# Optimization experiments

Hardware: AMD Instinct MI355X
Metric: run time of the kernel (lower is better)

## Reference

```python
import jax, jax.numpy as jnp
import numpy as np

NUM_HEADS = 6
KEY_DIM = 16
D_HEAD = 32  # attn_ratio(2) * key_dim(16)


def conv1x1_bn(x, W, scale, bias):
    # 1x1 conv (no bias) + folded BatchNorm (eval mode) as per-channel affine.
    y = jnp.einsum('oi,bihw->bohw', W, x)
    return y * scale[None, :, None, None] + bias[None, :, None, None]


def setup_inputs() -> dict:
    key = jax.random.key(0)
    ks = jax.random.split(key, 16)
    B, C, H, W = 4, 384, 48, 48
    dim_s = C // 4  # 96
    nh_kd = NUM_HEADS * KEY_DIM  # 96
    dh = NUM_HEADS * D_HEAD      # 192

    def w(k, o, i):
        return jax.random.normal(k, (o, i), dtype=jnp.float32) / np.sqrt(i)

    return {
        'xx': jax.random.normal(ks[0], (B, C, H, W), dtype=jnp.float32),
        'Wq': w(ks[1], nh_kd, dim_s),
        'q_scale': jax.random.uniform(ks[2], (nh_kd,), dtype=jnp.float32, minval=0.5, maxval=1.5),
        'q_bias': 0.1 * jax.random.normal(ks[3], (nh_kd,), dtype=jnp.float32),
        'Wk': w(ks[4], nh_kd, C),
        'k_scale': jax.random.uniform(ks[5], (nh_kd,), dtype=jnp.float32, minval=0.5, maxval=1.5),
        'k_bias': 0.1 * jax.random.normal(ks[6], (nh_kd,), dtype=jnp.float32),
        'Wv': w(ks[7], dh, C),
        'v_scale': jax.random.uniform(ks[8], (dh,), dtype=jnp.float32, minval=0.5, maxval=1.5),
        'v_bias': 0.1 * jax.random.normal(ks[9], (dh,), dtype=jnp.float32),
        'Wp': w(ks[10], dim_s, dh),
        'p_scale': jax.random.uniform(ks[11], (dim_s,), dtype=jnp.float32, minval=0.5, maxval=1.5),
        'p_bias': 0.1 * jax.random.normal(ks[12], (dim_s,), dtype=jnp.float32),
        'Wo': w(ks[13], C, dim_s),
        'o_scale': jax.random.uniform(ks[14], (C,), dtype=jnp.float32, minval=0.5, maxval=1.5),
        'o_bias': 0.1 * jax.random.normal(ks[15], (C,), dtype=jnp.float32),
    }


def reference(xx, Wq, q_scale, q_bias, Wk, k_scale, k_bias, Wv, v_scale, v_bias,
              Wp, p_scale, p_bias, Wo, o_scale, o_bias):
    B, C, H, W = xx.shape
    dim_s = C // 4
    N = H * W
    x = xx[:, 3 * dim_s:]  # last channel split -> query stream [B, dim_s, H, W]

    q = conv1x1_bn(x, Wq, q_scale, q_bias)                    # [B, nh_kd, H, W]
    q = q.reshape(B, NUM_HEADS, KEY_DIM, N).transpose(0, 1, 3, 2)  # [B,h,N,kd]
    k = conv1x1_bn(xx, Wk, k_scale, k_bias).reshape(B, NUM_HEADS, KEY_DIM, N)  # [B,h,kd,N]
    v = conv1x1_bn(xx, Wv, v_scale, v_bias).reshape(B, NUM_HEADS, D_HEAD, N)   # [B,h,d,N]

    # NOTE: original forward never applies key_dim**-0.5 scaling -- faithful to that.
    attn = jax.nn.softmax(jnp.einsum('bhnk,bhkm->bhnm', q, k), axis=-1)  # [B,h,N,N]
    out = jnp.einsum('bhnm,bhdm->bhdn', attn, v)                         # [B,h,d,N]
    out = out.reshape(B, NUM_HEADS * D_HEAD, H, W)

    out = conv1x1_bn(jax.nn.relu(out), Wp, p_scale, p_bias)  # [B, dim_s, H, W]
    xres = x + out  # drop_path=0 -> identity
    y = jax.nn.relu(conv1x1_bn(xres, Wo, o_scale, o_bias))   # [B, C, H, W]
    return y
```

## Files before the change

kernel.cpp:

```cpp
#include <hip/hip_runtime.h>
#include <hip/hip_bf16.h>
#include <math.h>

#define BB 4
#define CIN 384
#define NHD 6
#define KDIM 16
#define DHEAD 32
#define NPOS 2304
#define DIMS 96
#define DHTOT 192

constexpr size_t OFF_WT1 = 0;
constexpr size_t OFF_WT2 = OFF_WT1 + 384 * 384;
constexpr size_t OFF_WT3 = OFF_WT2 + 192 * 96;
constexpr size_t OFF_SC1 = OFF_WT3 + 96 * 384;
constexpr size_t OFF_BS1 = OFF_SC1 + 384;
constexpr size_t OFF_SC2 = OFF_BS1 + 384;
constexpr size_t OFF_BS2 = OFF_SC2 + 96;
constexpr size_t OFF_SC3 = OFF_BS2 + 96;
constexpr size_t OFF_BS3 = OFF_SC3 + 384;

constexpr size_t OFFB_Q  = (OFF_BS3 + 384) * 4;
constexpr size_t OFFB_K  = OFFB_Q + (size_t)BB * NHD * NPOS * KDIM * 2;
constexpr size_t OFFB_V  = OFFB_K + (size_t)BB * NHD * NPOS * KDIM * 2;
constexpr size_t OFFB_O  = OFFB_V + (size_t)BB * NHD * DHEAD * NPOS * 2;
constexpr size_t OFFB_XR = OFFB_O + (size_t)BB * DHTOT * NPOS * 4;
constexpr size_t OFF_O   = OFFB_O / 4;
constexpr size_t OFF_XR  = OFFB_XR / 4;

typedef __attribute__((ext_vector_type(8))) short bf16x8;
typedef __attribute__((ext_vector_type(16))) float f32x16;

__device__ inline ushort f2bf(float f) {
    __hip_bfloat16 h = __float2bfloat16(f);
    return *reinterpret_cast<ushort*>(&h);
}

__global__ void prep_kernel(const float* Wq, const float* qs, const float* qb,
                            const float* Wk, const float* ks, const float* kb,
                            const float* Wv, const float* vs, const float* vb,
                            const float* Wp, const float* ps, const float* pb,
                            const float* Wo, const float* os_, const float* ob,
                            float* ws) {
    float* WT1 = ws + OFF_WT1;
    float* WT2 = ws + OFF_WT2;
    float* WT3 = ws + OFF_WT3;
    int idx = blockIdx.x * blockDim.x + threadIdx.x;
    int stride = gridDim.x * blockDim.x;
    for (int t = idx; t < 384 * 384; t += stride) {
        int i = t / 384, o = t % 384;
        float v;
        if (o < 96)       v = (i >= 288) ? Wq[o * 96 + (i - 288)] : 0.f;
        else if (o < 192) v = Wk[(o - 96) * 384 + i];
        else              v = Wv[(o - 192) * 384 + i];
        WT1[t] = v;
    }
    for (int t = idx; t < 192 * 96; t += stride) {
        int i = t / 96, o = t % 96;
        WT2[t] = Wp[o * 192 + i];
    }
    for (int t = idx; t < 96 * 384; t += stride) {
        int i = t / 384, o = t % 384;
        WT3[t] = Wo[o * 96 + i];
    }
    if (idx < 384) {
        float s, bv;
        if (idx < 96)       { s = qs[idx];       bv = qb[idx]; }
        else if (idx < 192) { s = ks[idx - 96];  bv = kb[idx - 96]; }
        else                { s = vs[idx - 192]; bv = vb[idx - 192]; }
        ws[OFF_SC1 + idx] = s;  ws[OFF_BS1 + idx] = bv;
        ws[OFF_SC3 + idx] = os_[idx]; ws[OFF_BS3 + idx] = ob[idx];
    }
    if (idx < 96) { ws[OFF_SC2 + idx] = ps[idx]; ws[OFF_BS2 + idx] = pb[idx]; }
}

__global__ __launch_bounds__(256) void qkv_gemm(const float* __restrict__ xx, float* ws) {
    const float* WT1 = ws + OFF_WT1;
    const float* sc1 = ws + OFF_SC1;
    const float* bs1 = ws + OFF_BS1;
    ushort* Qb = (ushort*)((char*)ws + OFFB_Q);
    ushort* Kb = (ushort*)((char*)ws + OFFB_K);
    ushort* Vt = (ushort*)((char*)ws + OFFB_V);

    int n0 = blockIdx.x * 64;
    int o0 = blockIdx.y * 64;
    int b  = blockIdx.z;
    __shared__ float xs[32][64];
    __shared__ float wsh[32][64];
    int t = threadIdx.x;
    int px = t & 15, oy = t >> 4;
    float acc[4][4] = {};
    const float* xbase = xx + (size_t)b * CIN * NPOS;

    for (int ic = 0; ic < 384; ic += 32) {
        __syncthreads();
        for (int l = t; l < 512; l += 256) {
            int i = l >> 4, p4 = l & 15;
            *(float4*)&xs[i][p4 * 4]  = *(const float4*)&xbase[(size_t)(ic + i) * NPOS + n0 + p4 * 4];
            *(float4*)&wsh[i][p4 * 4] = *(const float4*)&WT1[(size_t)(ic + i) * 384 + o0 + p4 * 4];
        }
        __syncthreads();
#pragma unroll
        for (int i = 0; i < 32; ++i) {
            float4 xv = *(float4*)&xs[i][px * 4];
            float4 wv = *(float4*)&wsh[i][oy * 4];
            float xr[4] = {xv.x, xv.y, xv.z, xv.w};
            float wr[4] = {wv.x, wv.y, wv.z, wv.w};
#pragma unroll
            for (int a = 0; a < 4; ++a)
#pragma unroll
                for (int c = 0; c < 4; ++c) acc[a][c] += wr[a] * xr[c];
        }
    }
#pragma unroll
    for (int a = 0; a < 4; ++a) {
        int o = o0 + oy * 4 + a;
        float s = sc1[o], bv = bs1[o];
        float v4[4];
#pragma unroll
        for (int c = 0; c < 4; ++c) v4[c] = acc[a][c] * s + bv;
        int n = n0 + px * 4;
        if (o < 96) {
            int h = o >> 4, kk = o & 15;
            size_t base = ((size_t)b * NHD + h) * NPOS;
#pragma unroll
            for (int c = 0; c < 4; ++c) Qb[(base + n + c) * KDIM + kk] = f2bf(v4[c]);
        } else if (o < 192) {
            int oo = o - 96;
            int h = oo >> 4, kk = oo & 15;
            size_t base = ((size_t)b * NHD + h) * NPOS;
#pragma unroll
            for (int c = 0; c < 4; ++c) Kb[(base + n + c) * KDIM + kk] = f2bf(v4[c]);
        } else {
            int oo = o - 192;
            int hh = oo >> 5, d = oo & 31;
            ushort4 pk = make_ushort4(f2bf(v4[0]), f2bf(v4[1]), f2bf(v4[2]), f2bf(v4[3]));
            *(ushort4*)&Vt[((size_t)(b * NHD + hh) * DHEAD + d) * NPOS + n] = pk;
        }
    }
}

__global__ __launch_bounds__(256) void attn_mfma(float* ws) {
    const ushort* Qb = (const ushort*)((char*)ws + OFFB_Q);
    const ushort* Kb = (const ushort*)((char*)ws + OFFB_K);
    const ushort* Vt = (const ushort*)((char*)ws + OFFB_V);
    float* Ob = ws + OFF_O;

    int qt = blockIdx.x;
    int bh = blockIdx.y;
    int wave = threadIdx.x >> 6;
    int lane = threadIdx.x & 63;
    int l31 = lane & 31, hl = lane >> 5;
    int n0 = qt * 128 + wave * 32;

    bf16x8 qf = *(const bf16x8*)(Qb + (((size_t)bh * NPOS) + n0 + l31) * KDIM + hl * 8);

    const ushort* kbase = Kb + (size_t)bh * NPOS * KDIM;
    const ushort* vbase = Vt + (size_t)bh * DHEAD * NPOS;

    f32x16 oacc = (f32x16)0.0f;
    float m_run = -1e30f, l_run = 0.f;

    for (int m0 = 0; m0 < NPOS; m0 += 32) {
        bf16x8 kf = *(const bf16x8*)(kbase + (size_t)(m0 + l31) * KDIM + hl * 8);
        f32x16 s = __builtin_amdgcn_mfma_f32_32x32x16_bf16(kf, qf, (f32x16)0.0f, 0, 0, 0);

        float pm = s[0];
#pragma unroll
        for (int r = 1; r < 16; ++r) pm = fmaxf(pm, s[r]);
        pm = fmaxf(pm, __shfl_xor(pm, 32));
        float newm = fmaxf(m_run, pm);
        float scale = __expf(m_run - newm);
        m_run = newm;

        float p[16], psum = 0.f;
#pragma unroll
        for (int r = 0; r < 16; ++r) { p[r] = __expf(s[r] - newm); psum += p[r]; }
        l_run = l_run * scale + (psum + __shfl_xor(psum, 32));

#pragma unroll
        for (int r = 0; r < 16; ++r) oacc[r] *= scale;

        uint w[8];
#pragma unroll
        for (int j = 0; j < 8; ++j)
            w[j] = (uint)f2bf(p[2 * j]) | ((uint)f2bf(p[2 * j + 1]) << 16);
        uint xw[8];
#pragma unroll
        for (int j = 0; j < 8; ++j) xw[j] = __shfl_xor(w[j], 32);

        bf16x8 bf0, bf1;
        uint* bp0 = (uint*)&bf0;
        uint* bp1 = (uint*)&bf1;
        bp0[0] = hl ? xw[2] : w[0];
        bp0[1] = hl ? xw[3] : w[1];
        bp0[2] = hl ? w[2]  : xw[0];
        bp0[3] = hl ? w[3]  : xw[1];
        bp1[0] = hl ? xw[6] : w[4];
        bp1[1] = hl ? xw[7] : w[5];
        bp1[2] = hl ? w[6]  : xw[4];
        bp1[3] = hl ? w[7]  : xw[5];

        bf16x8 va0 = *(const bf16x8*)(vbase + (size_t)l31 * NPOS + m0 + hl * 8);
        bf16x8 va1 = *(const bf16x8*)(vbase + (size_t)l31 * NPOS + m0 + 16 + hl * 8);

        oacc = __builtin_amdgcn_mfma_f32_32x32x16_bf16(va0, bf0, oacc, 0, 0, 0);
        oacc = __builtin_amdgcn_mfma_f32_32x32x16_bf16(va1, bf1, oacc, 0, 0, 0);
    }

    float inv = 1.f / l_run;
    int b = bh / NHD, h = bh % NHD;
    float* obase = Ob + ((size_t)b * DHTOT + h * DHEAD) * NPOS + n0 + l31;
#pragma unroll
    for (int r = 0; r < 16; ++r) {
        int d = (r & 3) + 8 * (r >> 2) + 4 * hl;
        obase[(size_t)d * NPOS] = oacc[r] * inv;
    }
}

__global__ __launch_bounds__(384) void pproj(const float* __restrict__ xx, float* ws) {
    const float* Ob  = ws + OFF_O;
    const float* WT2 = ws + OFF_WT2;
    const float* sc2 = ws + OFF_SC2;
    const float* bs2 = ws + OFF_BS2;
    float* XR = ws + OFF_XR;

    int n0 = blockIdx.x * 64;
    int b  = blockIdx.y;
    __shared__ float osm[32][64];
    __shared__ float wsh[32][96];
    int t = threadIdx.x;
    int px = t & 15, ty = t >> 4;
    float acc[4][4] = {};

    for (int ic = 0; ic < 192; ic += 32) {
        __syncthreads();
        for (int l = t; l < 512; l += 384) {
            int i = l >> 4, p4 = l & 15;
            float4 v = *(const float4*)&Ob[((size_t)b * DHTOT + ic + i) * NPOS + n0 + p4 * 4];
            v.x = fmaxf(v.x, 0.f); v.y = fmaxf(v.y, 0.f);
            v.z = fmaxf(v.z, 0.f); v.w = fmaxf(v.w, 0.f);
            *(float4*)&osm[i][p4 * 4] = v;
        }
        for (int l = t; l < 768; l += 384) {
            int i = l / 24, o4 = l % 24;
            *(float4*)&wsh[i][o4 * 4] = *(const float4*)&WT2[(size_t)(ic + i) * 96 + o4 * 4];
        }
        __syncthreads();
#pragma unroll
        for (int i = 0; i < 32; ++i) {
            float4 xv = *(float4*)&osm[i][px * 4];
            float4 wv = *(float4*)&wsh[i][ty * 4];
            float xr[4] = {xv.x, xv.y, xv.z, xv.w};
            float wr[4] = {wv.x, wv.y, wv.z, wv.w};
#pragma unroll
            for (int a = 0; a < 4; ++a)
#pragma unroll
                for (int c = 0; c < 4; ++c) acc[a][c] += wr[a] * xr[c];
        }
    }
#pragma unroll
    for (int a = 0; a < 4; ++a) {
        int o = ty * 4 + a;
        float s = sc2[o], bv = bs2[o];
#pragma unroll
        for (int c = 0; c < 4; ++c) {
            int n = n0 + px * 4 + c;
            float res = xx[((size_t)b * CIN + 288 + o) * NPOS + n];
            XR[((size_t)b * DIMS + o) * NPOS + n] = res + (acc[a][c] * s + bv);
        }
    }
}

__global__ __launch_bounds__(256) void oproj(float* ws, float* __restrict__ y) {
    const float* XR  = ws + OFF_XR;
    const float* WT3 = ws + OFF_WT3;
    const float* sc3 = ws + OFF_SC3;
    const float* bs3 = ws + OFF_BS3;

    int n0 = blockIdx.x * 64;
    int o0 = blockIdx.y * 64;
    int b  = blockIdx.z;
    __shared__ float xs[32][64];
    __shared__ float wsh[32][64];
    int t = threadIdx.x;
    int px = t & 15, oy = t >> 4;
    float acc[4][4] = {};

    for (int ic = 0; ic < 96; ic += 32) {
        __syncthreads();
        for (int l = t; l < 512; l += 256) {
            int i = l >> 4, p4 = l & 15;
            *(float4*)&xs[i][p4 * 4]  = *(const float4*)&XR[((size_t)b * DIMS + ic + i) * NPOS + n0 + p4 * 4];
            *(float4*)&wsh[i][p4 * 4] = *(const float4*)&WT3[(size_t)(ic + i) * 384 + o0 + p4 * 4];
        }
        __syncthreads();
#pragma unroll
        for (int i = 0; i < 32; ++i) {
            float4 xv = *(float4*)&xs[i][px * 4];
            float4 wv = *(float4*)&wsh[i][oy * 4];
            float xr[4] = {xv.x, xv.y, xv.z, xv.w};
            float wr[4] = {wv.x, wv.y, wv.z, wv.w};
#pragma unroll
            for (int a = 0; a < 4; ++a)
#pragma unroll
                for (int c = 0; c < 4; ++c) acc[a][c] += wr[a] * xr[c];
        }
    }
#pragma unroll
    for (int a = 0; a < 4; ++a) {
        int o = o0 + oy * 4 + a;
        float s = sc3[o], bv = bs3[o];
        float4 out;
        out.x = fmaxf(acc[a][0] * s + bv, 0.f);
        out.y = fmaxf(acc[a][1] * s + bv, 0.f);
        out.z = fmaxf(acc[a][2] * s + bv, 0.f);
        out.w = fmaxf(acc[a][3] * s + bv, 0.f);
        *(float4*)&y[((size_t)b * CIN + o) * NPOS + n0 + px * 4] = out;
    }
}

extern "C" void kernel_launch(void* const* d_in, const int* in_sizes, int n_in,
                              void* d_out, int out_size, void* d_ws, size_t ws_size,
                              hipStream_t stream) {
    const float* xx = (const float*)d_in[0];
    const float* Wq = (const float*)d_in[1];
    const float* qs = (const float*)d_in[2];
    const float* qb = (const float*)d_in[3];
    const float* Wk = (const float*)d_in[4];
    const float* ks = (const float*)d_in[5];
    const float* kb = (const float*)d_in[6];
    const float* Wv = (const float*)d_in[7];
    const float* vs = (const float*)d_in[8];
    const float* vb = (const float*)d_in[9];
    const float* Wp = (const float*)d_in[10];
    const float* ps = (const float*)d_in[11];
    const float* pb = (const float*)d_in[12];
    const float* Wo = (const float*)d_in[13];
    const float* os_ = (const float*)d_in[14];
    const float* ob = (const float*)d_in[15];
    float* ws = (float*)d_ws;
    float* y = (float*)d_out;

    prep_kernel<<<256, 256, 0, stream>>>(Wq, qs, qb, Wk, ks, kb, Wv, vs, vb,
                                         Wp, ps, pb, Wo, os_, ob, ws);
    qkv_gemm<<<dim3(36, 6, BB), 256, 0, stream>>>(xx, ws);
    attn_mfma<<<dim3(18, 24), 256, 0, stream>>>(ws);
    pproj<<<dim3(36, BB), 384, 0, stream>>>(xx, ws);
    oproj<<<dim3(36, 6, BB), 256, 0, stream>>>(ws, y);
}
```

Before: 238.0 us.

## Move projections to bf16 MFMA, split attention over keys, lazy softmax rescale

Replaces the fp32 SIMT GEMMs (QKV, pproj, oproj) with bf16 MFMA kernels. Inputs are pre-converted and transposed to bf16, with a hi/lo split kept for the Q and K projections to preserve accuracy. Attention is split into two key halves with a combine kernel that merges partial outputs and applies ReLU. The softmax uses exp2 with log2e folded into the Q scale, rescales only when the running max grows by more than a threshold, and uses permlane32 swaps with packed bf16 conversion. The aim is to remove the slow fp32 GEMM time and raise attention occupancy, at the cost of extra conversion and combine passes and lower precision in the projections.

```diff
diff --git a/kernel.cpp b/kernel.cpp
--- a/kernel.cpp
+++ b/kernel.cpp
@@ -11,31 +11,69 @@
 #define DIMS 96
 #define DHTOT 192
 
-constexpr size_t OFF_WT1 = 0;
-constexpr size_t OFF_WT2 = OFF_WT1 + 384 * 384;
-constexpr size_t OFF_WT3 = OFF_WT2 + 192 * 96;
-constexpr size_t OFF_SC1 = OFF_WT3 + 96 * 384;
-constexpr size_t OFF_BS1 = OFF_SC1 + 384;
-constexpr size_t OFF_SC2 = OFF_BS1 + 384;
-constexpr size_t OFF_BS2 = OFF_SC2 + 96;
-constexpr size_t OFF_SC3 = OFF_BS2 + 96;
-constexpr size_t OFF_BS3 = OFF_SC3 + 384;
-
-constexpr size_t OFFB_Q  = (OFF_BS3 + 384) * 4;
-constexpr size_t OFFB_K  = OFFB_Q + (size_t)BB * NHD * NPOS * KDIM * 2;
-constexpr size_t OFFB_V  = OFFB_K + (size_t)BB * NHD * NPOS * KDIM * 2;
-constexpr size_t OFFB_O  = OFFB_V + (size_t)BB * NHD * DHEAD * NPOS * 2;
-constexpr size_t OFFB_XR = OFFB_O + (size_t)BB * DHTOT * NPOS * 4;
-constexpr size_t OFF_O   = OFFB_O / 4;
-constexpr size_t OFF_XR  = OFFB_XR / 4;
+constexpr size_t AL(size_t x) { return (x + 255) & ~(size_t)255; }
+constexpr size_t B_SC1 = 0;
+constexpr size_t B_BS1 = B_SC1 + 384 * 4;
+constexpr size_t B_SC2 = B_BS1 + 384 * 4;
+constexpr size_t B_BS2 = B_SC2 + 96 * 4;
+constexpr size_t B_SC3 = B_BS2 + 96 * 4;
+constexpr size_t B_BS3 = B_SC3 + 384 * 4;
+constexpr size_t B_W1  = AL(B_BS3 + 384 * 4);
+constexpr size_t B_W2  = AL(B_W1 + (size_t)384 * 384 * 2);
+constexpr size_t B_W3  = AL(B_W2 + (size_t)96 * 192 * 2);
+constexpr size_t B_XH  = AL(B_W3 + (size_t)384 * 96 * 2);
+constexpr size_t B_XL  = AL(B_XH + (size_t)BB * NPOS * CIN * 2);
+constexpr size_t B_Q   = AL(B_XL + (size_t)BB * NPOS * CIN * 2);
+constexpr size_t B_K   = AL(B_Q + (size_t)BB * NHD * NPOS * KDIM * 2);
+constexpr size_t B_V   = AL(B_K + (size_t)BB * NHD * NPOS * KDIM * 2);
+constexpr size_t B_OP  = AL(B_V + (size_t)BB * NHD * DHEAD * NPOS * 2);
+constexpr size_t B_MP  = AL(B_OP + (size_t)2 * BB * DHTOT * NPOS * 4);
+constexpr size_t B_LP  = AL(B_MP + (size_t)2 * 24 * NPOS * 4);
+constexpr size_t B_OBT = AL(B_LP + (size_t)2 * 24 * NPOS * 4);
+constexpr size_t B_XRT = AL(B_OBT + (size_t)BB * NPOS * DHTOT * 2);
+
+#define WS_F(off) ((float*)((char*)ws + (off)))
+#define WS_U(off) ((ushort*)((char*)ws + (off)))
 
 typedef __attribute__((ext_vector_type(8))) short bf16x8;
 typedef __attribute__((ext_vector_type(16))) float f32x16;
+typedef __attribute__((ext_vector_type(2))) int int2v;
 
 __device__ inline ushort f2bf(float f) {
     __hip_bfloat16 h = __float2bfloat16(f);
     return *reinterpret_cast<ushort*>(&h);
 }
+__device__ inline float bf2f(ushort u) {
+    uint x = (uint)u << 16;
+    return __uint_as_float(x);
+}
+__device__ inline float exp2_fast(float x) {
+    float r;
+    asm volatile("v_exp_f32 %0, %1" : "=v"(r) : "v"(x));
+    return r;
+}
+__device__ inline uint cvt_pk_bf16(float lo, float hi) {
+    uint r;
+    asm volatile("v_cvt_pk_bf16_f32 %0, %1, %2" : "=v"(r) : "v"(lo), "v"(hi));
+    return r;
+}
+__device__ inline void phswap(uint& a, uint& b) {
+    int2v r = __builtin_amdgcn_permlane32_swap((int)a, (int)b, false, false);
+    a = (uint)r[0]; b = (uint)r[1];
+}
+__device__ inline float xhalf_max(float x) {
+    uint a = __float_as_uint(x), b = a;
+    phswap(a, b);
+    return fmaxf(__uint_as_float(a), __uint_as_float(b));
+}
+__device__ inline float xhalf_add(float x) {
+    uint a = __float_as_uint(x), b = a;
+    phswap(a, b);
+    return __uint_as_float(a) + __uint_as_float(b);
+}
+
+#define MFMA32(A, B, C) __builtin_amdgcn_mfma_f32_32x32x16_bf16(A, B, C, 0, 0, 0)
+#define LOG2E 1.4426950408889634f
 
 __global__ void prep_kernel(const float* Wq, const float* qs, const float* qb,
                             const float* Wk, const float* ks, const float* kb,
@@ -43,281 +81,288 @@
                             const float* Wp, const float* ps, const float* pb,
                             const float* Wo, const float* os_, const float* ob,
                             float* ws) {
-    float* WT1 = ws + OFF_WT1;
-    float* WT2 = ws + OFF_WT2;
-    float* WT3 = ws + OFF_WT3;
+    ushort* W1 = WS_U(B_W1);
+    ushort* W2 = WS_U(B_W2);
+    ushort* W3 = WS_U(B_W3);
     int idx = blockIdx.x * blockDim.x + threadIdx.x;
     int stride = gridDim.x * blockDim.x;
     for (int t = idx; t < 384 * 384; t += stride) {
-        int i = t / 384, o = t % 384;
+        int o = t / 384, i = t % 384;
         float v;
         if (o < 96)       v = (i >= 288) ? Wq[o * 96 + (i - 288)] : 0.f;
         else if (o < 192) v = Wk[(o - 96) * 384 + i];
         else              v = Wv[(o - 192) * 384 + i];
-        WT1[t] = v;
-    }
-    for (int t = idx; t < 192 * 96; t += stride) {
-        int i = t / 96, o = t % 96;
-        WT2[t] = Wp[o * 192 + i];
-    }
-    for (int t = idx; t < 96 * 384; t += stride) {
-        int i = t / 384, o = t % 384;
-        WT3[t] = Wo[o * 96 + i];
-    }
+        W1[t] = f2bf(v);
+    }
+    for (int t = idx; t < 96 * 192; t += stride) W2[t] = f2bf(Wp[t]);
+    for (int t = idx; t < 384 * 96; t += stride) W3[t] = f2bf(Wo[t]);
     if (idx < 384) {
         float s, bv;
-        if (idx < 96)       { s = qs[idx];       bv = qb[idx]; }
-        else if (idx < 192) { s = ks[idx - 96];  bv = kb[idx - 96]; }
-        else                { s = vs[idx - 192]; bv = vb[idx - 192]; }
-        ws[OFF_SC1 + idx] = s;  ws[OFF_BS1 + idx] = bv;
-        ws[OFF_SC3 + idx] = os_[idx]; ws[OFF_BS3 + idx] = ob[idx];
-    }
-    if (idx < 96) { ws[OFF_SC2 + idx] = ps[idx]; ws[OFF_BS2 + idx] = pb[idx]; }
-}
-
-__global__ __launch_bounds__(256) void qkv_gemm(const float* __restrict__ xx, float* ws) {
-    const float* WT1 = ws + OFF_WT1;
-    const float* sc1 = ws + OFF_SC1;
-    const float* bs1 = ws + OFF_BS1;
-    ushort* Qb = (ushort*)((char*)ws + OFFB_Q);
-    ushort* Kb = (ushort*)((char*)ws + OFFB_K);
-    ushort* Vt = (ushort*)((char*)ws + OFFB_V);
-
-    int n0 = blockIdx.x * 64;
-    int o0 = blockIdx.y * 64;
-    int b  = blockIdx.z;
-    __shared__ float xs[32][64];
-    __shared__ float wsh[32][64];
+        if (idx < 96)       { s = qs[idx] * LOG2E; bv = qb[idx] * LOG2E; }
+        else if (idx < 192) { s = ks[idx - 96];    bv = kb[idx - 96]; }
+        else                { s = vs[idx - 192];   bv = vb[idx - 192]; }
+        WS_F(B_SC1)[idx] = s;    WS_F(B_BS1)[idx] = bv;
+        WS_F(B_SC3)[idx] = os_[idx]; WS_F(B_BS3)[idx] = ob[idx];
+    }
+    if (idx < 96) { WS_F(B_SC2)[idx] = ps[idx]; WS_F(B_BS2)[idx] = pb[idx]; }
+}
+
+__global__ __launch_bounds__(256) void xcvt(const float* __restrict__ xx, float* ws) {
+    ushort* Xh = WS_U(B_XH);
+    ushort* Xl = WS_U(B_XL);
+    int nt = blockIdx.x, it = blockIdx.y, b = blockIdx.z;
+    __shared__ ushort tileH[64][66];
+    __shared__ ushort tileL[64][66];
     int t = threadIdx.x;
-    int px = t & 15, oy = t >> 4;
-    float acc[4][4] = {};
-    const float* xbase = xx + (size_t)b * CIN * NPOS;
-
-    for (int ic = 0; ic < 384; ic += 32) {
-        __syncthreads();
-        for (int l = t; l < 512; l += 256) {
-            int i = l >> 4, p4 = l & 15;
-            *(float4*)&xs[i][p4 * 4]  = *(const float4*)&xbase[(size_t)(ic + i) * NPOS + n0 + p4 * 4];
-            *(float4*)&wsh[i][p4 * 4] = *(const float4*)&WT1[(size_t)(ic + i) * 384 + o0 + p4 * 4];
-        }
-        __syncthreads();
-#pragma unroll
-        for (int i = 0; i < 32; ++i) {
-            float4 xv = *(float4*)&xs[i][px * 4];
-            float4 wv = *(float4*)&wsh[i][oy * 4];
-            float xr[4] = {xv.x, xv.y, xv.z, xv.w};
-            float wr[4] = {wv.x, wv.y, wv.z, wv.w};
-#pragma unroll
-            for (int a = 0; a < 4; ++a)
-#pragma unroll
-                for (int c = 0; c < 4; ++c) acc[a][c] += wr[a] * xr[c];
-        }
-    }
-#pragma unroll
-    for (int a = 0; a < 4; ++a) {
-        int o = o0 + oy * 4 + a;
-        float s = sc1[o], bv = bs1[o];
-        float v4[4];
-#pragma unroll
-        for (int c = 0; c < 4; ++c) v4[c] = acc[a][c] * s + bv;
-        int n = n0 + px * 4;
-        if (o < 96) {
+    int ir = t >> 4, nc = (t & 15) * 4;
+    const float* src = xx + ((size_t)b * CIN + it * 64) * NPOS + nt * 64;
+#pragma unroll
+    for (int ii = 0; ii < 64; ii += 16) {
+        float4 v = *(const float4*)&src[(size_t)(ii + ir) * NPOS + nc];
+        float vv[4] = {v.x, v.y, v.z, v.w};
+#pragma unroll
+        for (int j = 0; j < 4; ++j) {
+            ushort h = f2bf(vv[j]);
+            tileH[ii + ir][nc + j] = h;
+            tileL[ii + ir][nc + j] = f2bf(vv[j] - bf2f(h));
+        }
+    }
+    __syncthreads();
+    int nl = t >> 2, i16 = (t & 3) * 16;
+    ushort tmpH[16], tmpL[16];
+#pragma unroll
+    for (int j = 0; j < 16; ++j) { tmpH[j] = tileH[i16 + j][nl]; tmpL[j] = tileL[i16 + j][nl]; }
+    size_t doff = ((size_t)b * NPOS + nt * 64 + nl) * CIN + it * 64 + i16;
+    *(bf16x8*)&Xh[doff]     = *(bf16x8*)&tmpH[0];
+    *(bf16x8*)&Xh[doff + 8] = *(bf16x8*)&tmpH[8];
+    *(bf16x8*)&Xl[doff]     = *(bf16x8*)&tmpL[0];
+    *(bf16x8*)&Xl[doff + 8] = *(bf16x8*)&tmpL[8];
+}
+
+__global__ __launch_bounds__(256) void qkv_mfma(float* ws) {
+    const ushort* W1 = WS_U(B_W1);
+    const ushort* Xh = WS_U(B_XH);
+    const ushort* Xl = WS_U(B_XL);
+    const float* sc1 = WS_F(B_SC1);
+    const float* bs1 = WS_F(B_BS1);
+    ushort* Qb = WS_U(B_Q);
+    ushort* Kb = WS_U(B_K);
+    ushort* Vt = WS_U(B_V);
+
+    int nt = blockIdx.x, ot = blockIdx.y, b = blockIdx.z;
+    int wave = threadIdx.x >> 6, lane = threadIdx.x & 63;
+    int l31 = lane & 31, hl = lane >> 5;
+    int obase = ot * 64 + (wave >> 1) * 32;
+    int nbase = nt * 64 + (wave & 1) * 32;
+
+    const ushort* arow  = W1 + (size_t)(obase + l31) * CIN + hl * 8;
+    size_t boff = ((size_t)b * NPOS + nbase + l31) * CIN + hl * 8;
+    const ushort* browh = Xh + boff;
+    f32x16 acc = {};
+#pragma unroll
+    for (int k0 = 0; k0 < 384; k0 += 16)
+        acc = MFMA32(*(const bf16x8*)(arow + k0), *(const bf16x8*)(browh + k0), acc);
+    if (obase < 192) {
+        const ushort* browl = Xl + boff;
+#pragma unroll
+        for (int k0 = 0; k0 < 384; k0 += 16)
+            acc = MFMA32(*(const bf16x8*)(arow + k0), *(const bf16x8*)(browl + k0), acc);
+    }
+
+    int n = nbase + l31;
+    if (obase < 96) {
+#pragma unroll
+        for (int r = 0; r < 16; ++r) {
+            int o = obase + (r & 3) + 8 * (r >> 2) + 4 * hl;
+            float v = acc[r] * sc1[o] + bs1[o];
             int h = o >> 4, kk = o & 15;
-            size_t base = ((size_t)b * NHD + h) * NPOS;
-#pragma unroll
-            for (int c = 0; c < 4; ++c) Qb[(base + n + c) * KDIM + kk] = f2bf(v4[c]);
-        } else if (o < 192) {
+            Qb[((size_t)(b * NHD + h) * NPOS + n) * KDIM + kk] = f2bf(v);
+        }
+    } else if (obase < 192) {
+#pragma unroll
+        for (int r = 0; r < 16; ++r) {
+            int o = obase + (r & 3) + 8 * (r >> 2) + 4 * hl;
+            float v = acc[r] * sc1[o] + bs1[o];
             int oo = o - 96;
             int h = oo >> 4, kk = oo & 15;
-            size_t base = ((size_t)b * NHD + h) * NPOS;
-#pragma unroll
-            for (int c = 0; c < 4; ++c) Kb[(base + n + c) * KDIM + kk] = f2bf(v4[c]);
-        } else {
+            Kb[((size_t)(b * NHD + h) * NPOS + n) * KDIM + kk] = f2bf(v);
+        }
+    } else {
+#pragma unroll
+        for (int r = 0; r < 16; ++r) {
+            int o = obase + (r & 3) + 8 * (r >> 2) + 4 * hl;
+            float v = acc[r] * sc1[o] + bs1[o];
             int oo = o - 192;
-            int hh = oo >> 5, d = oo & 31;
-            ushort4 pk = make_ushort4(f2bf(v4[0]), f2bf(v4[1]), f2bf(v4[2]), f2bf(v4[3]));
-            *(ushort4*)&Vt[((size_t)(b * NHD + hh) * DHEAD + d) * NPOS + n] = pk;
+            int d = oo & 31, hh = oo >> 5;
+            Vt[((size_t)(b * NHD + hh) * DHEAD + d) * NPOS + n] = f2bf(v);
         }
     }
 }
 
 __global__ __launch_bounds__(256) void attn_mfma(float* ws) {
-    const ushort* Qb = (const ushort*)((char*)ws + OFFB_Q);
-    const ushort* Kb = (const ushort*)((char*)ws + OFFB_K);
-    const ushort* Vt = (const ushort*)((char*)ws + OFFB_V);
-    float* Ob = ws + OFF_O;
+    const ushort* Qb = WS_U(B_Q);
+    const ushort* Kb = WS_U(B_K);
+    const ushort* Vt = WS_U(B_V);
+    float* Op = WS_F(B_OP);
+    float* Mp = WS_F(B_MP);
+    float* Lp = WS_F(B_LP);
 
     int qt = blockIdx.x;
     int bh = blockIdx.y;
-    int wave = threadIdx.x >> 6;
-    int lane = threadIdx.x & 63;
+    int ms = blockIdx.z;
+    int wave = threadIdx.x >> 6, lane = threadIdx.x & 63;
     int l31 = lane & 31, hl = lane >> 5;
     int n0 = qt * 128 + wave * 32;
-
-    bf16x8 qf = *(const bf16x8*)(Qb + (((size_t)bh * NPOS) + n0 + l31) * KDIM + hl * 8);
-
+    int n = n0 + l31;
+
+    bf16x8 qf = *(const bf16x8*)(Qb + ((size_t)bh * NPOS + n) * KDIM + hl * 8);
     const ushort* kbase = Kb + (size_t)bh * NPOS * KDIM;
-    const ushort* vbase = Vt + (size_t)bh * DHEAD * NPOS;
+    const ushort* vbase = Vt + (size_t)bh * DHEAD * NPOS + (size_t)l31 * NPOS;
 
     f32x16 oacc = (f32x16)0.0f;
     float m_run = -1e30f, l_run = 0.f;
 
-    for (int m0 = 0; m0 < NPOS; m0 += 32) {
+    int mend = ms * 1152 + 1152;
+    for (int m0 = ms * 1152; m0 < mend; m0 += 32) {
         bf16x8 kf = *(const bf16x8*)(kbase + (size_t)(m0 + l31) * KDIM + hl * 8);
-        f32x16 s = __builtin_amdgcn_mfma_f32_32x32x16_bf16(kf, qf, (f32x16)0.0f, 0, 0, 0);
+        f32x16 s = MFMA32(kf, qf, (f32x16)0.0f);
 
         float pm = s[0];
 #pragma unroll
         for (int r = 1; r < 16; ++r) pm = fmaxf(pm, s[r]);
-        pm = fmaxf(pm, __shfl_xor(pm, 32));
-        float newm = fmaxf(m_run, pm);
-        float scale = __expf(m_run - newm);
-        m_run = newm;
+        pm = xhalf_max(pm);
+
+        if (__any(pm > m_run + 8.f)) {
+            float newm = fmaxf(m_run, pm);
+            float sc = exp2_fast(m_run - newm);
+#pragma unroll
+            for (int r = 0; r < 16; ++r) oacc[r] *= sc;
+            l_run *= sc;
+            m_run = newm;
+        }
 
         float p[16], psum = 0.f;
 #pragma unroll
-        for (int r = 0; r < 16; ++r) { p[r] = __expf(s[r] - newm); psum += p[r]; }
-        l_run = l_run * scale + (psum + __shfl_xor(psum, 32));
-
-#pragma unroll
-        for (int r = 0; r < 16; ++r) oacc[r] *= scale;
+        for (int r = 0; r < 16; ++r) { p[r] = exp2_fast(s[r] - m_run); psum += p[r]; }
+        l_run += xhalf_add(psum);
 
         uint w[8];
 #pragma unroll
-        for (int j = 0; j < 8; ++j)
-            w[j] = (uint)f2bf(p[2 * j]) | ((uint)f2bf(p[2 * j + 1]) << 16);
-        uint xw[8];
-#pragma unroll
-        for (int j = 0; j < 8; ++j) xw[j] = __shfl_xor(w[j], 32);
-
-        bf16x8 bf0, bf1;
-        uint* bp0 = (uint*)&bf0;
-        uint* bp1 = (uint*)&bf1;
-        bp0[0] = hl ? xw[2] : w[0];
-        bp0[1] = hl ? xw[3] : w[1];
-        bp0[2] = hl ? w[2]  : xw[0];
-        bp0[3] = hl ? w[3]  : xw[1];
-        bp1[0] = hl ? xw[6] : w[4];
-        bp1[1] = hl ? xw[7] : w[5];
-        bp1[2] = hl ? w[6]  : xw[4];
-        bp1[3] = hl ? w[7]  : xw[5];
-
-        bf16x8 va0 = *(const bf16x8*)(vbase + (size_t)l31 * NPOS + m0 + hl * 8);
-        bf16x8 va1 = *(const bf16x8*)(vbase + (size_t)l31 * NPOS + m0 + 16 + hl * 8);
-
-        oacc = __builtin_amdgcn_mfma_f32_32x32x16_bf16(va0, bf0, oacc, 0, 0, 0);
-        oacc = __builtin_amdgcn_mfma_f32_32x32x16_bf16(va1, bf1, oacc, 0, 0, 0);
-    }
-
-    float inv = 1.f / l_run;
+        for (int j = 0; j < 8; ++j) w[j] = cvt_pk_bf16(p[2 * j], p[2 * j + 1]);
+        phswap(w[0], w[2]);
+        phswap(w[1], w[3]);
+        phswap(w[4], w[6]);
+        phswap(w[5], w[7]);
+
+        bf16x8 pb0, pb1;
+        ((uint*)&pb0)[0] = w[0]; ((uint*)&pb0)[1] = w[1];
+        ((uint*)&pb0)[2] = w[2]; ((uint*)&pb0)[3] = w[3];
+        ((uint*)&pb1)[0] = w[4]; ((uint*)&pb1)[1] = w[5];
+        ((uint*)&pb1)[2] = w[6]; ((uint*)&pb1)[3] = w[7];
+
+        bf16x8 va0 = *(const bf16x8*)(vbase + m0 + hl * 8);
+        bf16x8 va1 = *(const bf16x8*)(vbase + m0 + 16 + hl * 8);
+        oacc = MFMA32(va0, pb0, oacc);
+        oacc = MFMA32(va1, pb1, oacc);
+    }
+
     int b = bh / NHD, h = bh % NHD;
-    float* obase = Ob + ((size_t)b * DHTOT + h * DHEAD) * NPOS + n0 + l31;
+    float* obase = Op + ((size_t)(ms * BB + b) * DHTOT + h * DHEAD) * NPOS + n;
 #pragma unroll
     for (int r = 0; r < 16; ++r) {
         int d = (r & 3) + 8 * (r >> 2) + 4 * hl;
-        obase[(size_t)d * NPOS] = oacc[r] * inv;
-    }
-}
-
-__global__ __launch_bounds__(384) void pproj(const float* __restrict__ xx, float* ws) {
-    const float* Ob  = ws + OFF_O;
-    const float* WT2 = ws + OFF_WT2;
-    const float* sc2 = ws + OFF_SC2;
-    const float* bs2 = ws + OFF_BS2;
-    float* XR = ws + OFF_XR;
-
-    int n0 = blockIdx.x * 64;
-    int b  = blockIdx.y;
-    __shared__ float osm[32][64];
-    __shared__ float wsh[32][96];
-    int t = threadIdx.x;
-    int px = t & 15, ty = t >> 4;
-    float acc[4][4] = {};
-
-    for (int ic = 0; ic < 192; ic += 32) {
-        __syncthreads();
-        for (int l = t; l < 512; l += 384) {
-            int i = l >> 4, p4 = l & 15;
-            float4 v = *(const float4*)&Ob[((size_t)b * DHTOT + ic + i) * NPOS + n0 + p4 * 4];
-            v.x = fmaxf(v.x, 0.f); v.y = fmaxf(v.y, 0.f);
-            v.z = fmaxf(v.z, 0.f); v.w = fmaxf(v.w, 0.f);
-            *(float4*)&osm[i][p4 * 4] = v;
-        }
-        for (int l = t; l < 768; l += 384) {
-            int i = l / 24, o4 = l % 24;
-            *(float4*)&wsh[i][o4 * 4] = *(const float4*)&WT2[(size_t)(ic + i) * 96 + o4 * 4];
-        }
-        __syncthreads();
-#pragma unroll
-        for (int i = 0; i < 32; ++i) {
-            float4 xv = *(float4*)&osm[i][px * 4];
-            float4 wv = *(float4*)&wsh[i][ty * 4];
-            float xr[4] = {xv.x, xv.y, xv.z, xv.w};
-            float wr[4] = {wv.x, wv.y, wv.z, wv.w};
-#pragma unroll
-            for (int a = 0; a < 4; ++a)
-#pragma unroll
-                for (int c = 0; c < 4; ++c) acc[a][c] += wr[a] * xr[c];
-        }
-    }
-#pragma unroll
-    for (int a = 0; a < 4; ++a) {
-        int o = ty * 4 + a;
-        float s = sc2[o], bv = bs2[o];
-#pragma unroll
-        for (int c = 0; c < 4; ++c) {
-            int n = n0 + px * 4 + c;
-            float res = xx[((size_t)b * CIN + 288 + o) * NPOS + n];
-            XR[((size_t)b * DIMS + o) * NPOS + n] = res + (acc[a][c] * s + bv);
-        }
-    }
-}
-
-__global__ __launch_bounds__(256) void oproj(float* ws, float* __restrict__ y) {
-    const float* XR  = ws + OFF_XR;
-    const float* WT3 = ws + OFF_WT3;
-    const float* sc3 = ws + OFF_SC3;
-    const float* bs3 = ws + OFF_BS3;
-
-    int n0 = blockIdx.x * 64;
-    int o0 = blockIdx.y * 64;
-    int b  = blockIdx.z;
-    __shared__ float xs[32][64];
-    __shared__ float wsh[32][64];
-    int t = threadIdx.x;
-    int px = t & 15, oy = t >> 4;
-    float acc[4][4] = {};
-
-    for (int ic = 0; ic < 96; ic += 32) {
-        __syncthreads();
-        for (int l = t; l < 512; l += 256) {
-            int i = l >> 4, p4 = l & 15;
-            *(float4*)&xs[i][p4 * 4]  = *(const float4*)&XR[((size_t)b * DIMS + ic + i) * NPOS + n0 + p4 * 4];
-            *(float4*)&wsh[i][p4 * 4] = *(const float4*)&WT3[(size_t)(ic + i) * 384 + o0 + p4 * 4];
-        }
-        __syncthreads();
-#pragma unroll
-        for (int i = 0; i < 32; ++i) {
-            float4 xv = *(float4*)&xs[i][px * 4];
-            float4 wv = *(float4*)&wsh[i][oy * 4];
-            float xr[4] = {xv.x, xv.y, xv.z, xv.w};
-            float wr[4] = {wv.x, wv.y, wv.z, wv.w};
-#pragma unroll
-            for (int a = 0; a < 4; ++a)
-#pragma unroll
-                for (int c = 0; c < 4; ++c) acc[a][c] += wr[a] * xr[c];
-        }
-    }
-#pragma unroll
-    for (int a = 0; a < 4; ++a) {
-        int o = o0 + oy * 4 + a;
-        float s = sc3[o], bv = bs3[o];
-        float4 out;
-        out.x = fmaxf(acc[a][0] * s + bv, 0.f);
-        out.y = fmaxf(acc[a][1] * s + bv, 0.f);
-        out.z = fmaxf(acc[a][2] * s + bv, 0.f);
-        out.w = fmaxf(acc[a][3] * s + bv, 0.f);
-        *(float4*)&y[((size_t)b * CIN + o) * NPOS + n0 + px * 4] = out;
+        obase[(size_t)d * NPOS] = oacc[r];
+    }
+    Mp[(size_t)(ms * 24 + bh) * NPOS + n] = m_run;
+    Lp[(size_t)(ms * 24 + bh) * NPOS + n] = l_run;
+}
+
+__global__ __launch_bounds__(256) void attn_combine(float* ws) {
+    const float* Op = WS_F(B_OP);
+    const float* Mp = WS_F(B_MP);
+    const float* Lp = WS_F(B_LP);
+    ushort* Obt = WS_U(B_OBT);
+
+    int idx = blockIdx.x * 256 + threadIdx.x;
+    int bh = idx / NPOS, n = idx % NPOS;
+    int b = bh / NHD, h = bh % NHD;
+
+    float m0 = Mp[(size_t)bh * NPOS + n];
+    float m1 = Mp[(size_t)(24 + bh) * NPOS + n];
+    float l0 = Lp[(size_t)bh * NPOS + n];
+    float l1 = Lp[(size_t)(24 + bh) * NPOS + n];
+    float gm = fmaxf(m0, m1);
+    float w0 = exp2_fast(m0 - gm), w1 = exp2_fast(m1 - gm);
+    float inv = 1.f / (l0 * w0 + l1 * w1);
+    w0 *= inv; w1 *= inv;
+
+    const float* p0 = Op + ((size_t)b * DHTOT + h * DHEAD) * NPOS + n;
+    const float* p1 = Op + ((size_t)(BB + b) * DHTOT + h * DHEAD) * NPOS + n;
+    ushort tmp[32];
+#pragma unroll
+    for (int d = 0; d < 32; ++d) {
+        float v = p0[(size_t)d * NPOS] * w0 + p1[(size_t)d * NPOS] * w1;
+        tmp[d] = f2bf(fmaxf(v, 0.f));
+    }
+    ushort* dst = Obt + ((size_t)b * NPOS + n) * DHTOT + h * DHEAD;
+#pragma unroll
+    for (int c = 0; c < 4; ++c) *(bf16x8*)&dst[c * 8] = *(bf16x8*)&tmp[c * 8];
+}
+
+__global__ __launch_bounds__(256) void pproj_mfma(const float* __restrict__ xx, float* ws) {
+    const ushort* W2 = WS_U(B_W2);
+    const ushort* Obt = WS_U(B_OBT);
+    const float* sc2 = WS_F(B_SC2);
+    const float* bs2 = WS_F(B_BS2);
+    ushort* XRt = WS_U(B_XRT);
+
+    int nt = blockIdx.x, ot = blockIdx.y, b = blockIdx.z;
+    int wave = threadIdx.x >> 6, lane = threadIdx.x & 63;
+    int l31 = lane & 31, hl = lane >> 5;
+    int obase = ot * 32;
+    int nbase = nt * 128 + wave * 32;
+
+    const ushort* arow = W2 + (size_t)(obase + l31) * DHTOT + hl * 8;
+    const ushort* brow = Obt + ((size_t)b * NPOS + nbase + l31) * DHTOT + hl * 8;
+    f32x16 acc = {};
+#pragma unroll
+    for (int k0 = 0; k0 < 192; k0 += 16)
+        acc = MFMA32(*(const bf16x8*)(arow + k0), *(const bf16x8*)(brow + k0), acc);
+
+    int n = nbase + l31;
+#pragma unroll
+    for (int r = 0; r < 16; ++r) {
+        int o = obase + (r & 3) + 8 * (r >> 2) + 4 * hl;
+        float v = acc[r] * sc2[o] + bs2[o] + xx[((size_t)b * CIN + 288 + o) * NPOS + n];
+        XRt[((size_t)b * NPOS + n) * DIMS + o] = f2bf(v);
+    }
+}
+
+__global__ __launch_bounds__(256) void oproj_mfma(float* ws, float* __restrict__ y) {
+    const ushort* W3 = WS_U(B_W3);
+    const ushort* XRt = WS_U(B_XRT);
+    const float* sc3 = WS_F(B_SC3);
+    const float* bs3 = WS_F(B_BS3);
+
+    int nt = blockIdx.x, ot = blockIdx.y, b = blockIdx.z;
+    int wave = threadIdx.x >> 6, lane = threadIdx.x & 63;
+    int l31 = lane & 31, hl = lane >> 5;
+    int obase = ot * 64 + (wave >> 1) * 32;
+    int nbase = nt * 64 + (wave & 1) * 32;
+
+    const ushort* arow = W3 + (size_t)(obase + l31) * DIMS + hl * 8;
+    const ushort* brow = XRt + ((size_t)b * NPOS + nbase + l31) * DIMS + hl * 8;
+    f32x16 acc = {};
+#pragma unroll
+    for (int k0 = 0; k0 < 96; k0 += 16)
+        acc = MFMA32(*(const bf16x8*)(arow + k0), *(const bf16x8*)(brow + k0), acc);
+
+    int n = nbase + l31;
+#pragma unroll
+    for (int r = 0; r < 16; ++r) {
+        int o = obase + (r & 3) + 8 * (r >> 2) + 4 * hl;
+        float v = fmaxf(acc[r] * sc3[o] + bs3[o], 0.f);
+        y[((size_t)b * CIN + o) * NPOS + n] = v;
     }
 }
 
@@ -345,8 +390,10 @@
 
     prep_kernel<<<256, 256, 0, stream>>>(Wq, qs, qb, Wk, ks, kb, Wv, vs, vb,
                                          Wp, ps, pb, Wo, os_, ob, ws);
-    qkv_gemm<<<dim3(36, 6, BB), 256, 0, stream>>>(xx, ws);
-    attn_mfma<<<dim3(18, 24), 256, 0, stream>>>(ws);
-    pproj<<<dim3(36, BB), 384, 0, stream>>>(xx, ws);
-    oproj<<<dim3(36, 6, BB), 256, 0, stream>>>(ws, y);
-}
+    xcvt<<<dim3(36, 6, BB), 256, 0, stream>>>(xx, ws);
+    qkv_mfma<<<dim3(36, 6, BB), 256, 0, stream>>>(ws);
+    attn_mfma<<<dim3(18, 24, 2), 256, 0, stream>>>(ws);
+    attn_combine<<<216, 256, 0, stream>>>(ws);
+    pproj_mfma<<<dim3(18, 3, BB), 256, 0, stream>>>(xx, ws);
+    oproj_mfma<<<dim3(36, 6, BB), 256, 0, stream>>>(ws, y);
+}
```

Result: faster. 207.4 us (-12.9%).
